# Kernel tuning notes

Measured on AMD Instinct MI355X. Metric: run time of the kernel, lower is better.

Reference implementation:

```python
import jax, jax.numpy as jnp
import numpy as np

D_MODEL = 1024
N_HEADS = 16
D_K = D_MODEL // N_HEADS


def setup_inputs() -> dict:
    key = jax.random.key(0)
    ks = jax.random.split(key, 6)
    B, T = 4, 2048
    x = jax.random.normal(ks[0], (B, T, D_MODEL), dtype=jnp.float32)
    # additive causal mask: 0 on/below diagonal, -inf above
    neg = jnp.float32(-1e9)
    attn_mask = jnp.where(jnp.tril(jnp.ones((T, T), dtype=bool)), 0.0, neg).astype(jnp.float32)
    s_in = 1.0 / np.sqrt(D_MODEL)
    Wqkv = jax.random.normal(ks[1], (D_MODEL, 3 * D_MODEL), dtype=jnp.float32) * s_in
    bqkv = jnp.zeros((3 * D_MODEL,), dtype=jnp.float32)
    Wout = jax.random.normal(ks[2], (D_MODEL, D_MODEL), dtype=jnp.float32) * s_in
    bout = jnp.zeros((D_MODEL,), dtype=jnp.float32)
    return {"x": x, "attn_mask": attn_mask, "Wqkv": Wqkv, "bqkv": bqkv,
            "Wout": Wout, "bout": bout}


def reference(x, attn_mask, Wqkv, bqkv, Wout, bout):
    B, T, _ = x.shape
    qkv = x @ Wqkv + bqkv                                  # [B,T,3*D]
    qkv = qkv.reshape(B, T, 3, N_HEADS, D_K)
    qkv = jnp.transpose(qkv, (2, 0, 3, 1, 4))              # [3,B,H,T,d_k]
    q, k, v = qkv[0], qkv[1], qkv[2]
    scores = jnp.einsum('bhqd,bhkd->bhqk', q, k) / jnp.sqrt(jnp.float32(D_K))
    scores = scores + attn_mask                            # broadcast [T,T]
    probs = jax.nn.softmax(scores, axis=-1)
    attn_out = jnp.einsum('bhqk,bhkd->bhqd', probs, v)     # [B,H,T,d_k]
    attn_out = jnp.transpose(attn_out, (0, 2, 1, 3)).reshape(B, T, D_MODEL)
    return attn_out @ Wout + bout
```

## Files before the change

kernel.cpp:

```cpp
#include <hip/hip_runtime.h>
#include <hip/hip_bf16.h>
#include <stdint.h>

typedef __attribute__((ext_vector_type(8))) short short8;
typedef __attribute__((ext_vector_type(4))) short short4v;
typedef __attribute__((ext_vector_type(4))) float f32x4;
typedef __attribute__((ext_vector_type(4))) int   i32x4;

#define MFMA16(a, b, c) __builtin_amdgcn_mfma_f32_16x16x32_bf16((a), (b), (c), 0, 0, 0)

static __device__ __forceinline__ short f2bf(float f) {
    union { float f; uint32_t i; } v; v.f = f;
    uint32_t r = v.i + 0x7fffu + ((v.i >> 16) & 1u);
    return (short)(r >> 16);
}

static __device__ __forceinline__ int cvtpk(float a, float b) {
    int r;
    asm("v_cvt_pk_bf16_f32 %0, %1, %2" : "=v"(r) : "v"(a), "v"(b));
    return r;
}

__global__ void conv_f32_bf16(const float* __restrict__ in, short* __restrict__ out, int n4) {
    int i = blockIdx.x * blockDim.x + threadIdx.x;
    int stride = gridDim.x * blockDim.x;
    for (; i < n4; i += stride) {
        f32x4 v = *(const f32x4*)(in + (size_t)i * 4);
        short4v o;
        o[0] = f2bf(v[0]); o[1] = f2bf(v[1]); o[2] = f2bf(v[2]); o[3] = f2bf(v[3]);
        *(short4v*)(out + (size_t)i * 4) = o;
    }
}

__global__ void conv_transpose(const float* __restrict__ W, short* __restrict__ Wt, int R, int C) {
    __shared__ float tile[32][33];
    int c0 = blockIdx.x * 32;
    int r0 = blockIdx.y * 32;
    int tx = threadIdx.x;
    int ty = threadIdx.y;
    for (int j = 0; j < 4; ++j) {
        int r = ty * 4 + j;
        tile[r][tx] = W[(size_t)(r0 + r) * C + c0 + tx];
    }
    __syncthreads();
    for (int j = 0; j < 4; ++j) {
        int c = ty * 4 + j;
        Wt[(size_t)(c0 + c) * R + r0 + tx] = f2bf(tile[tx][c]);
    }
}

__global__ __launch_bounds__(256) void gemm_qkv(
    const short* __restrict__ A, const short* __restrict__ Bt,
    const float* __restrict__ bias,
    short* __restrict__ Qg, short* __restrict__ Kg, short* __restrict__ Vg)
{
    const int K = 1024;
    __shared__ short As[128 * 32];
    __shared__ short Bs[128 * 32];
    const int tid = threadIdx.x, lane = tid & 63, wid = tid >> 6;
    const int wr = wid >> 1, wc = wid & 1;
    const int m0 = blockIdx.y * 128, n0 = blockIdx.x * 128;
    const int l15 = lane & 15, l4 = lane >> 4;

    f32x4 acc[4][4] = {};

    int rowS[2], ugS[2];
    for (int t = 0; t < 2; ++t) {
        int c = tid + t * 256;
        rowS[t] = c >> 2;
        ugS[t] = (c & 3) ^ ((rowS[t] >> 1) & 3);
    }
    int offA[4], offB[4];
    for (int f = 0; f < 4; ++f) {
        int ra = wr * 64 + f * 16 + l15;
        offA[f] = ra * 32 + ((l4 ^ ((ra >> 1) & 3)) * 8);
        int rb = wc * 64 + f * 16 + l15;
        offB[f] = rb * 32 + ((l4 ^ ((rb >> 1) & 3)) * 8);
    }

    for (int k0 = 0; k0 < K; k0 += 32) {
        __syncthreads();
        for (int t = 0; t < 2; ++t) {
            const short* ga = A  + (size_t)(m0 + rowS[t]) * K + k0 + ugS[t] * 8;
            const short* gb = Bt + (size_t)(n0 + rowS[t]) * K + k0 + ugS[t] * 8;
            short* la = As + (t * 256 + wid * 64) * 8;
            short* lb = Bs + (t * 256 + wid * 64) * 8;
            __builtin_amdgcn_global_load_lds((const __attribute__((address_space(1))) void*)ga,
                                             (__attribute__((address_space(3))) void*)la, 16, 0, 0);
            __builtin_amdgcn_global_load_lds((const __attribute__((address_space(1))) void*)gb,
                                             (__attribute__((address_space(3))) void*)lb, 16, 0, 0);
        }
        __syncthreads();
        short8 a[4], b[4];
        for (int f = 0; f < 4; ++f) a[f] = *(const short8*)&As[offA[f]];
        for (int f = 0; f < 4; ++f) b[f] = *(const short8*)&Bs[offB[f]];
        for (int mf = 0; mf < 4; ++mf)
            for (int nf = 0; nf < 4; ++nf)
                acc[mf][nf] = MFMA16(a[mf], b[nf], acc[mf][nf]);
    }

    for (int mf = 0; mf < 4; ++mf) {
        int grow_base = m0 + wr * 64 + mf * 16 + l4 * 4;
        for (int nf = 0; nf < 4; ++nf) {
            int gcol = n0 + wc * 64 + nf * 16 + l15;
            float bb = bias[gcol];
            int which = gcol >> 10, rem = gcol & 1023;
            int h = rem >> 6, d = rem & 63;
            for (int r = 0; r < 4; ++r) {
                int grow = grow_base + r;
                int b = grow >> 11, t = grow & 2047;
                int bh = (b << 4) + h;
                float val = acc[mf][nf][r] + bb;
                if (which == 0) val *= 0.18033688011112042f;
                short bv = f2bf(val);
                if (which == 0)      Qg[((size_t)bh * 2048 + t) * 64 + d] = bv;
                else if (which == 1) Kg[((size_t)bh * 2048 + t) * 64 + d] = bv;
                else {
                    int k6 = t & 63;
                    int pos = (k6 & 32) + ((k6 & 12) << 1) + ((k6 & 16) >> 2) + (k6 & 3);
                    Vg[((size_t)bh * 64 + d) * 2048 + (t & ~63) + pos] = bv;
                }
            }
        }
    }
}

__global__ __launch_bounds__(256) void attn_kernel(
    const short* __restrict__ Qg, const short* __restrict__ Kg, const short* __restrict__ Vg,
    short* __restrict__ AO)
{
    const int tid = threadIdx.x, lane = tid & 63, wid = tid >> 6;
    const int l15 = lane & 15, l4 = lane >> 4;
    const int bp = blockIdx.x;
    const int xcd = bp & 7, slot = bp >> 3;
    const int bh = xcd * 8 + (slot >> 3);
    const int iblk = slot & 7;
    const int pr = iblk * 4 + wid;
    const short* Qh = Qg + (size_t)bh * 2048 * 64;
    const short* Kh = Kg + (size_t)bh * 2048 * 64;
    const short* Vh = Vg + (size_t)bh * 64 * 2048;
    const int b = bh >> 4, head = bh & 15;

    for (int half = 0; half < 2; ++half) {
        const int s = half ? (63 - pr) : pr;
        const int q0 = s * 32;
        const int nt = (s >> 1) + 1;

        short8 qf[2][2];
        #pragma unroll
        for (int h = 0; h < 2; ++h)
            #pragma unroll
            for (int c = 0; c < 2; ++c)
                qf[h][c] = *(const short8*)&Qh[(size_t)(q0 + h * 16 + l15) * 64 + c * 32 + l4 * 8];

        f32x4 o[2][4] = {};
        float lsum[2] = { 0.f, 0.f };

        for (int j = 0; j < nt; ++j) {
            const int kv0 = j * 64;
            const bool diag = (j == nt - 1);
            short8 kb[4][2], vb[4][2];
            #pragma unroll
            for (int kf = 0; kf < 4; ++kf)
                #pragma unroll
                for (int c = 0; c < 2; ++c)
                    kb[kf][c] = *(const short8*)&Kh[(size_t)(kv0 + kf * 16 + l15) * 64 + c * 32 + l4 * 8];
            #pragma unroll
            for (int df = 0; df < 4; ++df)
                #pragma unroll
                for (int c = 0; c < 2; ++c)
                    vb[df][c] = *(const short8*)&Vh[(size_t)(df * 16 + l15) * 2048 + kv0 + c * 32 + l4 * 8];

            #pragma unroll
            for (int h = 0; h < 2; ++h) {
                f32x4 sf[4];
                #pragma unroll
                for (int kf = 0; kf < 4; ++kf) {
                    f32x4 z = {};
                    z = MFMA16(kb[kf][0], qf[h][0], z);
                    z = MFMA16(kb[kf][1], qf[h][1], z);
                    sf[kf] = z;
                }
                const int gq = q0 + h * 16 + l15;
                int w[4][2];
                #pragma unroll
                for (int kf = 0; kf < 4; ++kf) {
                    float pf[4];
                    #pragma unroll
                    for (int r = 0; r < 4; ++r) {
                        float v = sf[kf][r];
                        if (diag && (kv0 + kf * 16 + l4 * 4 + r) > gq) v = -1e9f;
                        float pp = exp2f(v);
                        lsum[h] += pp;
                        pf[r] = pp;
                    }
                    w[kf][0] = cvtpk(pf[0], pf[1]);
                    w[kf][1] = cvtpk(pf[2], pf[3]);
                }
                union { i32x4 i; short8 s8; } pa0, pa1;
                pa0.i[0] = w[0][0]; pa0.i[1] = w[0][1]; pa0.i[2] = w[1][0]; pa0.i[3] = w[1][1];
                pa1.i[0] = w[2][0]; pa1.i[1] = w[2][1]; pa1.i[2] = w[3][0]; pa1.i[3] = w[3][1];
                #pragma unroll
                for (int df = 0; df < 4; ++df) {
                    o[h][df] = MFMA16(pa0.s8, vb[df][0], o[h][df]);
                    o[h][df] = MFMA16(pa1.s8, vb[df][1], o[h][df]);
                }
            }
        }

        #pragma unroll
        for (int h = 0; h < 2; ++h) {
            lsum[h] += __shfl_xor(lsum[h], 16, 64);
            lsum[h] += __shfl_xor(lsum[h], 32, 64);
        }

        #pragma unroll
        for (int h = 0; h < 2; ++h)
            #pragma unroll
            for (int r = 0; r < 4; ++r) {
                float inv = 1.0f / __shfl(lsum[h], l4 * 4 + r, 64);
                size_t grow = (size_t)b * 2048 + q0 + h * 16 + l4 * 4 + r;
                #pragma unroll
                for (int df = 0; df < 4; ++df)
                    AO[grow * 1024 + head * 64 + df * 16 + l15] = f2bf(o[h][df][r] * inv);
            }
    }
}

__global__ __launch_bounds__(256) void gemm_out(
    const short* __restrict__ A, const short* __restrict__ Bt,
    const float* __restrict__ bias, float* __restrict__ out)
{
    const int K = 1024;
    __shared__ short As[128 * 32];
    __shared__ short Bs[128 * 32];
    const int tid = threadIdx.x, lane = tid & 63, wid = tid >> 6;
    const int wr = wid >> 1, wc = wid & 1;
    const int m0 = blockIdx.y * 128, n0 = blockIdx.x * 128;
    const int l15 = lane & 15, l4 = lane >> 4;

    f32x4 acc[4][4] = {};

    int rowS[2], ugS[2];
    for (int t = 0; t < 2; ++t) {
        int c = tid + t * 256;
        rowS[t] = c >> 2;
        ugS[t] = (c & 3) ^ ((rowS[t] >> 1) & 3);
    }
    int offA[4], offB[4];
    for (int f = 0; f < 4; ++f) {
        int ra = wr * 64 + f * 16 + l15;
        offA[f] = ra * 32 + ((l4 ^ ((ra >> 1) & 3)) * 8);
        int rb = wc * 64 + f * 16 + l15;
        offB[f] = rb * 32 + ((l4 ^ ((rb >> 1) & 3)) * 8);
    }

    for (int k0 = 0; k0 < K; k0 += 32) {
        __syncthreads();
        for (int t = 0; t < 2; ++t) {
            const short* ga = A  + (size_t)(m0 + rowS[t]) * K + k0 + ugS[t] * 8;
            const short* gb = Bt + (size_t)(n0 + rowS[t]) * K + k0 + ugS[t] * 8;
            short* la = As + (t * 256 + wid * 64) * 8;
            short* lb = Bs + (t * 256 + wid * 64) * 8;
            __builtin_amdgcn_global_load_lds((const __attribute__((address_space(1))) void*)ga,
                                             (__attribute__((address_space(3))) void*)la, 16, 0, 0);
            __builtin_amdgcn_global_load_lds((const __attribute__((address_space(1))) void*)gb,
                                             (__attribute__((address_space(3))) void*)lb, 16, 0, 0);
        }
        __syncthreads();
        short8 a[4], b[4];
        for (int f = 0; f < 4; ++f) a[f] = *(const short8*)&As[offA[f]];
        for (int f = 0; f < 4; ++f) b[f] = *(const short8*)&Bs[offB[f]];
        for (int mf = 0; mf < 4; ++mf)
            for (int nf = 0; nf < 4; ++nf)
                acc[mf][nf] = MFMA16(a[mf], b[nf], acc[mf][nf]);
    }

    for (int mf = 0; mf < 4; ++mf) {
        int grow_base = m0 + wr * 64 + mf * 16 + l4 * 4;
        for (int nf = 0; nf < 4; ++nf) {
            int gcol = n0 + wc * 64 + nf * 16 + l15;
            float bb = bias[gcol];
            for (int r = 0; r < 4; ++r) {
                int grow = grow_base + r;
                out[(size_t)grow * 1024 + gcol] = acc[mf][nf][r] + bb;
            }
        }
    }
}

extern "C" void kernel_launch(void* const* d_in, const int* in_sizes, int n_in,
                              void* d_out, int out_size, void* d_ws, size_t ws_size,
                              hipStream_t stream) {
    (void)in_sizes; (void)n_in; (void)out_size; (void)ws_size;
    const float* x    = (const float*)d_in[0];
    const float* Wqkv = (const float*)d_in[2];
    const float* bqkv = (const float*)d_in[3];
    const float* Wout = (const float*)d_in[4];
    const float* bout = (const float*)d_in[5];
    float* out = (float*)d_out;

    char* ws = (char*)d_ws;
    short* xb    = (short*)(ws);
    short* WqkvT = (short*)(ws + (16ull << 20));
    short* WoutT = (short*)(ws + (22ull << 20));
    short* Qg    = (short*)(ws + (24ull << 20));
    short* Kg    = (short*)(ws + (40ull << 20));
    short* Vg    = (short*)(ws + (56ull << 20));
    short* AO    = xb;

    conv_f32_bf16<<<2048, 256, 0, stream>>>(x, xb, 8192 * 1024 / 4);
    conv_transpose<<<dim3(3072 / 32, 1024 / 32), dim3(32, 8), 0, stream>>>(Wqkv, WqkvT, 1024, 3072);
    conv_transpose<<<dim3(1024 / 32, 1024 / 32), dim3(32, 8), 0, stream>>>(Wout, WoutT, 1024, 1024);
    gemm_qkv<<<dim3(24, 64), 256, 0, stream>>>(xb, WqkvT, bqkv, Qg, Kg, Vg);
    attn_kernel<<<512, 256, 0, stream>>>(Qg, Kg, Vg, AO);
    gemm_out<<<dim3(8, 64), 256, 0, stream>>>(AO, WoutT, bout, out);
}
```

Before: 341.9 us.

## Stage K/V tiles in LDS with double-buffered async loads in attention

The attention kernel now has each block own one 64-row query tile, with its four waves sharing K and V tiles. Those tiles are staged into swizzled, double-buffered shared memory through global_load_lds, replacing per-wave direct global loads. The grid grows from 512 to 2048 blocks, and longer causal tiles are scheduled first, replacing the old paired-half load balancing inside each wave. The aim is to cut redundant global K/V traffic and overlap loads with MFMA work, at the cost of a block barrier on every iteration and some load imbalance across blocks.

```diff
diff --git a/kernel.cpp b/kernel.cpp
--- a/kernel.cpp
+++ b/kernel.cpp
@@ -32,7 +32,7 @@
     }
 }
 
-__global__ void conv_transpose(const float* __restrict__ W, short* __restrict__ Wt, int R, int C) {
+__global__ void conv_transpose2(const float* __restrict__ W, short* __restrict__ Wt, int R, int C) {
     __shared__ float tile[32][33];
     int c0 = blockIdx.x * 32;
     int r0 = blockIdx.y * 32;
@@ -129,102 +129,122 @@
     const short* __restrict__ Qg, const short* __restrict__ Kg, const short* __restrict__ Vg,
     short* __restrict__ AO)
 {
+    __shared__ __align__(16) short Ks[2][4096];
+    __shared__ __align__(16) short Vs[2][4096];
     const int tid = threadIdx.x, lane = tid & 63, wid = tid >> 6;
     const int l15 = lane & 15, l4 = lane >> 4;
     const int bp = blockIdx.x;
     const int xcd = bp & 7, slot = bp >> 3;
-    const int bh = xcd * 8 + (slot >> 3);
-    const int iblk = slot & 7;
-    const int pr = iblk * 4 + wid;
+    const int bh = xcd * 8 + (slot >> 5);
+    const int u  = 31 - (slot & 31);
     const short* Qh = Qg + (size_t)bh * 2048 * 64;
     const short* Kh = Kg + (size_t)bh * 2048 * 64;
     const short* Vh = Vg + (size_t)bh * 64 * 2048;
     const int b = bh >> 4, head = bh & 15;
-
-    for (int half = 0; half < 2; ++half) {
-        const int s = half ? (63 - pr) : pr;
-        const int q0 = s * 32;
-        const int nt = (s >> 1) + 1;
-
-        short8 qf[2][2];
-        #pragma unroll
-        for (int h = 0; h < 2; ++h)
+    const int q0 = u * 64;
+    const int nt = u + 1;
+
+#define STAGE(JJ, BB) do {                                                                       \
+    const int kv0_ = (JJ) * 64;                                                                  \
+    _Pragma("unroll")                                                                            \
+    for (int i_ = 0; i_ < 2; ++i_) {                                                             \
+        int L_ = i_ * 4096 + wid * 1024 + lane * 16;                       \
+        int G_ = L_ ^ (((L_ >> 7) & 7) << 4);                                    \
+        const char* ksrc = (const char*)Kh + (size_t)kv0_ * 128 + G_;                            \
+        short* kdst = &Ks[BB][0] + (i_ * 2048 + wid * 512);                                      \
+        __builtin_amdgcn_global_load_lds((const __attribute__((address_space(1))) void*)ksrc,    \
+                                         (__attribute__((address_space(3))) void*)kdst, 16, 0, 0);\
+        const char* vsrc = (const char*)Vh + (size_t)(G_ >> 7) * 4096 + (size_t)kv0_ * 2 + (G_ & 127);\
+        short* vdst = &Vs[BB][0] + (i_ * 2048 + wid * 512);                                      \
+        __builtin_amdgcn_global_load_lds((const __attribute__((address_space(1))) void*)vsrc,    \
+                                         (__attribute__((address_space(3))) void*)vdst, 16, 0, 0);\
+    }                                                                                            \
+} while (0)
+
+    short8 qf[2];
+    #pragma unroll
+    for (int c = 0; c < 2; ++c)
+        qf[c] = *(const short8*)&Qh[(size_t)(q0 + wid * 16 + l15) * 64 + c * 32 + l4 * 8];
+
+    f32x4 o[4] = {};
+    float lsum = 0.f;
+    const int gq = q0 + wid * 16 + l15;
+
+    STAGE(0, 0);
+    __syncthreads();
+
+    int cur = 0;
+    for (int j = 0; j < nt; ++j) {
+        if (j + 1 < nt) STAGE(j + 1, cur ^ 1);
+        const int kv0 = j * 64;
+        const bool diag = (j == nt - 1);
+
+        short8 kb[4][2], vb[4][2];
+        #pragma unroll
+        for (int kf = 0; kf < 4; ++kf)
             #pragma unroll
-            for (int c = 0; c < 2; ++c)
-                qf[h][c] = *(const short8*)&Qh[(size_t)(q0 + h * 16 + l15) * 64 + c * 32 + l4 * 8];
-
-        f32x4 o[2][4] = {};
-        float lsum[2] = { 0.f, 0.f };
-
-        for (int j = 0; j < nt; ++j) {
-            const int kv0 = j * 64;
-            const bool diag = (j == nt - 1);
-            short8 kb[4][2], vb[4][2];
+            for (int c = 0; c < 2; ++c) {
+                int rowK = kf * 16 + l15;
+                int A = rowK * 128 + c * 64 + l4 * 16;
+                kb[kf][c] = *(const short8*)((const char*)&Ks[cur][0] + (A ^ ((rowK & 7) << 4)));
+            }
+        #pragma unroll
+        for (int df = 0; df < 4; ++df)
             #pragma unroll
-            for (int kf = 0; kf < 4; ++kf)
-                #pragma unroll
-                for (int c = 0; c < 2; ++c)
-                    kb[kf][c] = *(const short8*)&Kh[(size_t)(kv0 + kf * 16 + l15) * 64 + c * 32 + l4 * 8];
-            #pragma unroll
-            for (int df = 0; df < 4; ++df)
-                #pragma unroll
-                for (int c = 0; c < 2; ++c)
-                    vb[df][c] = *(const short8*)&Vh[(size_t)(df * 16 + l15) * 2048 + kv0 + c * 32 + l4 * 8];
-
-            #pragma unroll
-            for (int h = 0; h < 2; ++h) {
-                f32x4 sf[4];
-                #pragma unroll
-                for (int kf = 0; kf < 4; ++kf) {
-                    f32x4 z = {};
-                    z = MFMA16(kb[kf][0], qf[h][0], z);
-                    z = MFMA16(kb[kf][1], qf[h][1], z);
-                    sf[kf] = z;
-                }
-                const int gq = q0 + h * 16 + l15;
-                int w[4][2];
-                #pragma unroll
-                for (int kf = 0; kf < 4; ++kf) {
-                    float pf[4];
-                    #pragma unroll
-                    for (int r = 0; r < 4; ++r) {
-                        float v = sf[kf][r];
-                        if (diag && (kv0 + kf * 16 + l4 * 4 + r) > gq) v = -1e9f;
-                        float pp = exp2f(v);
-                        lsum[h] += pp;
-                        pf[r] = pp;
-                    }
-                    w[kf][0] = cvtpk(pf[0], pf[1]);
-                    w[kf][1] = cvtpk(pf[2], pf[3]);
-                }
-                union { i32x4 i; short8 s8; } pa0, pa1;
-                pa0.i[0] = w[0][0]; pa0.i[1] = w[0][1]; pa0.i[2] = w[1][0]; pa0.i[3] = w[1][1];
-                pa1.i[0] = w[2][0]; pa1.i[1] = w[2][1]; pa1.i[2] = w[3][0]; pa1.i[3] = w[3][1];
-                #pragma unroll
-                for (int df = 0; df < 4; ++df) {
-                    o[h][df] = MFMA16(pa0.s8, vb[df][0], o[h][df]);
-                    o[h][df] = MFMA16(pa1.s8, vb[df][1], o[h][df]);
-                }
-            }
-        }
-
-        #pragma unroll
-        for (int h = 0; h < 2; ++h) {
-            lsum[h] += __shfl_xor(lsum[h], 16, 64);
-            lsum[h] += __shfl_xor(lsum[h], 32, 64);
-        }
-
-        #pragma unroll
-        for (int h = 0; h < 2; ++h)
+            for (int c = 0; c < 2; ++c) {
+                int rowV = df * 16 + l15;
+                int A = rowV * 128 + c * 64 + l4 * 16;
+                vb[df][c] = *(const short8*)((const char*)&Vs[cur][0] + (A ^ ((rowV & 7) << 4)));
+            }
+
+        f32x4 sf[4];
+        #pragma unroll
+        for (int kf = 0; kf < 4; ++kf) {
+            f32x4 z = {};
+            z = MFMA16(kb[kf][0], qf[0], z);
+            z = MFMA16(kb[kf][1], qf[1], z);
+            sf[kf] = z;
+        }
+        int w[4][2];
+        #pragma unroll
+        for (int kf = 0; kf < 4; ++kf) {
+            float pf[4];
             #pragma unroll
             for (int r = 0; r < 4; ++r) {
-                float inv = 1.0f / __shfl(lsum[h], l4 * 4 + r, 64);
-                size_t grow = (size_t)b * 2048 + q0 + h * 16 + l4 * 4 + r;
-                #pragma unroll
-                for (int df = 0; df < 4; ++df)
-                    AO[grow * 1024 + head * 64 + df * 16 + l15] = f2bf(o[h][df][r] * inv);
-            }
-    }
+                float v = sf[kf][r];
+                if (diag && (kv0 + kf * 16 + l4 * 4 + r) > gq) v = -1e9f;
+                float pp = exp2f(v);
+                lsum += pp;
+                pf[r] = pp;
+            }
+            w[kf][0] = cvtpk(pf[0], pf[1]);
+            w[kf][1] = cvtpk(pf[2], pf[3]);
+        }
+        union { i32x4 i; short8 s8; } pa0, pa1;
+        pa0.i[0] = w[0][0]; pa0.i[1] = w[0][1]; pa0.i[2] = w[1][0]; pa0.i[3] = w[1][1];
+        pa1.i[0] = w[2][0]; pa1.i[1] = w[2][1]; pa1.i[2] = w[3][0]; pa1.i[3] = w[3][1];
+        #pragma unroll
+        for (int df = 0; df < 4; ++df) {
+            o[df] = MFMA16(pa0.s8, vb[df][0], o[df]);
+            o[df] = MFMA16(pa1.s8, vb[df][1], o[df]);
+        }
+
+        __syncthreads();
+        cur ^= 1;
+    }
+
+    lsum += __shfl_xor(lsum, 16, 64);
+    lsum += __shfl_xor(lsum, 32, 64);
+
+    #pragma unroll
+    for (int r = 0; r < 4; ++r) {
+        float inv = 1.0f / __shfl(lsum, l4 * 4 + r, 64);
+        size_t grow = (size_t)b * 2048 + q0 + wid * 16 + l4 * 4 + r;
+        #pragma unroll
+        for (int df = 0; df < 4; ++df)
+            AO[grow * 1024 + head * 64 + df * 16 + l15] = f2bf(o[df][r] * inv);
+    }
+#undef STAGE
 }
 
 __global__ __launch_bounds__(256) void gemm_out(
@@ -310,9 +330,9 @@
     short* AO    = xb;
 
     conv_f32_bf16<<<2048, 256, 0, stream>>>(x, xb, 8192 * 1024 / 4);
-    conv_transpose<<<dim3(3072 / 32, 1024 / 32), dim3(32, 8), 0, stream>>>(Wqkv, WqkvT, 1024, 3072);
-    conv_transpose<<<dim3(1024 / 32, 1024 / 32), dim3(32, 8), 0, stream>>>(Wout, WoutT, 1024, 1024);
+    conv_transpose2<<<dim3(3072 / 32, 1024 / 32), dim3(32, 8), 0, stream>>>(Wqkv, WqkvT, 1024, 3072);
+    conv_transpose2<<<dim3(1024 / 32, 1024 / 32), dim3(32, 8), 0, stream>>>(Wout, WoutT, 1024, 1024);
     gemm_qkv<<<dim3(24, 64), 256, 0, stream>>>(xb, WqkvT, bqkv, Qg, Kg, Vg);
-    attn_kernel<<<512, 256, 0, stream>>>(Qg, Kg, Vg, AO);
+    attn_kernel<<<2048, 256, 0, stream>>>(Qg, Kg, Vg, AO);
     gemm_out<<<dim3(8, 64), 256, 0, stream>>>(AO, WoutT, bout, out);
 }
```

New measurement: 312.6 us. 1.09x faster.
